# Kernel tuning notes

Hardware: AMD Instinct MI355X
Metric: run time of the kernel (lower is better)

Reference implementation:

```python
import jax, jax.numpy as jnp
import numpy as np

B, C, H, W = 4, 128, 64, 64
THITA = 1e-4


def conv1x1(x, w, b):
    # 1x1 conv + bias + ReLU; x:[B,Cin,H,W], w:[Cout,Cin], b:[Cout]
    return jax.nn.relu(jnp.einsum('bihw,oi->bohw', x, w) + b[None, :, None, None])


_CONV_SPECS = [
    ('neighbor', 2 * C, 4),
    ('pro_key', C, C), ('pro_val', C, C),
    ('lat_key', C, C), ('lat_val', C, C),
    ('tmp1', C, 2 * C),
    ('now1', C, 2),
    ('now_key', C, C), ('now_val', C, C),
    ('q', C, C), ('k', C, C), ('v', C, C),
]


def setup_inputs() -> dict:
    key = jax.random.key(0)
    ks = jax.random.split(key, 1 + 2 * len(_CONV_SPECS))
    inp = {'event': jax.random.normal(ks[0], (B, 6, H, W), dtype=jnp.float32)}
    i = 1
    for name, o, c in _CONV_SPECS:
        s = 1.0 / np.sqrt(c)
        inp['w_' + name] = jax.random.uniform(ks[i], (o, c), minval=-s, maxval=s, dtype=jnp.float32)
        inp['b_' + name] = jax.random.uniform(ks[i + 1], (o,), minval=-s, maxval=s, dtype=jnp.float32)
        i += 2
    return inp


def reference(event, w_neighbor, b_neighbor, w_pro_key, b_pro_key, w_pro_val, b_pro_val,
              w_lat_key, b_lat_key, w_lat_val, b_lat_val, w_tmp1, b_tmp1,
              w_now1, b_now1, w_now_key, b_now_key, w_now_val, b_now_val,
              w_q, b_q, w_k, b_k, w_v, b_v):
    pro, now, lat = event[:, 0:2], event[:, 2:4], event[:, 4:6]
    neigh = conv1x1(jnp.concatenate([pro, lat], axis=1), w_neighbor, b_neighbor)  # [B,2C,H,W]
    pro_key = conv1x1(neigh[:, :C], w_pro_key, b_pro_key)
    pro_val = conv1x1(neigh[:, C:], w_pro_val, b_pro_val)
    lat_key = conv1x1(neigh[:, :C], w_lat_key, b_lat_key)
    lat_val = conv1x1(neigh[:, C:], w_lat_val, b_lat_val)
    # NOTE: source applies conv_tmp1 (shared weights) to both key and val paths
    key_n = conv1x1(jnp.concatenate([pro_key, lat_key], axis=1), w_tmp1, b_tmp1)
    val_n = conv1x1(jnp.concatenate([pro_val, lat_val], axis=1), w_tmp1, b_tmp1)
    now_f = conv1x1(now, w_now1, b_now1)
    now_key = conv1x1(now_f, w_now_key, b_now_key)
    now_val = conv1x1(now_f, w_now_val, b_now_val)
    N = H * W
    q = conv1x1(key_n, w_q, b_q).reshape(B, C, N)          # proj_query pre-permute
    k = conv1x1(now_key, w_k, b_k).reshape(B, C, N)        # [B,C,N]
    attn = jax.nn.softmax(jnp.einsum('bcn,bcm->bnm', q, k), axis=-1)  # [B,N,N]
    v = conv1x1(val_n, w_v, b_v).reshape(B, C, N)
    out = jnp.einsum('bcm,bnm->bcn', v, attn).reshape(B, C, H, W)
    return THITA * out + now_val
```

## Files before the change

### kernel.cpp

```cpp
#include <hip/hip_runtime.h>

#define B_ 4
#define C_ 128
#define N_ 4096
#define LOG2E 1.44269504088896340736f

typedef __attribute__((ext_vector_type(8))) __bf16 bf16x8;
typedef __attribute__((ext_vector_type(16))) float f32x16;

#define SWZ(n) (((n) & 15) << 4)

__device__ __forceinline__ unsigned short cvb(float x) {
    return __builtin_bit_cast(unsigned short, (__bf16)x);
}
__device__ __forceinline__ unsigned pk2(float lo, float hi) {
    return (unsigned)cvb(lo) | ((unsigned)cvb(hi) << 16);
}
__device__ __forceinline__ float bfu(unsigned short u) {
    return __builtin_bit_cast(float, (unsigned)u << 16);
}
__device__ __forceinline__ float fexp2(float x) {
#if __has_builtin(__builtin_amdgcn_exp2f)
    return __builtin_amdgcn_exp2f(x);
#else
    float r;
    asm("v_exp_f32 %0, %1" : "=v"(r) : "v"(x));
    return r;
#endif
}
__device__ inline void gload_lds16(const void* g, void* l) {
    __builtin_amdgcn_global_load_lds(
        (const __attribute__((address_space(1))) unsigned int*)g,
        (__attribute__((address_space(3))) unsigned int*)l, 16, 0, 0);
}
__device__ __forceinline__ void plswapf(float& a, float& b) {
    asm volatile("v_permlane32_swap_b32 %0, %1" : "+v"(a), "+v"(b));
}
__device__ __forceinline__ void plswapu(unsigned& a, unsigned& b) {
    asm volatile("v_permlane32_swap_b32 %0, %1" : "+v"(a), "+v"(b));
}

__global__ __launch_bounds__(256) void k_wcvt(
        const float* pk, const float* lk, const float* pv, const float* lv,
        const float* t1, const float* nk, const float* nv,
        const float* q, const float* k, const float* v,
        const float* bpk, const float* blk, const float* bpv, const float* blv,
        const float* bnk, const float* bnv,
        unsigned short* Wk, unsigned short* Wv, unsigned short* Wt1,
        unsigned short* Wnow, unsigned short* Wq, unsigned short* Wkk,
        unsigned short* Wvv, float* bck, float* bcv, float* bcn) {
    int i = blockIdx.x * 256 + threadIdx.x;
    if      (i < 16384)  Wk[i] = cvb(pk[i]);
    else if (i < 32768)  Wk[i] = cvb(lk[i - 16384]);
    else if (i < 49152)  Wv[i - 32768] = cvb(pv[i - 32768]);
    else if (i < 65536)  Wv[i - 32768] = cvb(lv[i - 49152]);
    else if (i < 98304)  Wt1[i - 65536] = cvb(t1[i - 65536]);
    else if (i < 114688) Wnow[i - 98304] = cvb(nk[i - 98304]);
    else if (i < 131072) Wnow[i - 98304] = cvb(nv[i - 114688]);
    else if (i < 147456) Wq[i - 131072] = cvb(q[i - 131072]);
    else if (i < 163840) Wkk[i - 147456] = cvb(k[i - 147456]);
    else if (i < 180224) Wvv[i - 163840] = cvb(v[i - 163840]);
    else if (i < 180480) { int j = i - 180224; bck[j] = j < 128 ? bpk[j] : blk[j - 128]; }
    else if (i < 180736) { int j = i - 180480; bcv[j] = j < 128 ? bpv[j] : blv[j - 128]; }
    else if (i < 180992) { int j = i - 180736; bcn[j] = j < 128 ? bnk[j] : bnv[j - 128]; }
}

template<int KSTEPS, int ROWB>
__device__ __forceinline__ f32x16 gtile(const char* Ab, int aChBase,
        const unsigned short* W, int Wld, int wrow0, int nsub, int nl, int h) {
    f32x16 acc;
    #pragma unroll
    for (int r = 0; r < 16; ++r) acc[r] = 0.f;
    int n = nsub * 32 + nl;
    const char* arow = Ab + n * ROWB;
    const unsigned short* wrow = W + (size_t)(wrow0 + nl) * Wld + h * 8;
    #pragma unroll
    for (int kk = 0; kk < KSTEPS; ++kk) {
        bf16x8 a = *(const bf16x8*)(arow + ((aChBase + kk * 32 + h * 16) ^ SWZ(n)));
        bf16x8 wf = *(const bf16x8*)(wrow + kk * 16);
        acc = __builtin_amdgcn_mfma_f32_32x32x16_bf16(a, wf, acc, 0, 0, 0);
    }
    return acc;
}

__device__ __forceinline__ void epi_lds(char* dst, int rowB, f32x16 acc,
        const float* bias, int m0, int nsub, int nl, int h) {
    int m = m0 + nl;
    float bs = bias[m];
    #pragma unroll
    for (int r = 0; r < 16; ++r) {
        int n = nsub * 32 + (r & 3) + 8 * (r >> 2) + 4 * h;
        *(unsigned short*)(dst + n * rowB + ((m * 2) ^ SWZ(n))) =
            cvb(fmaxf(acc[r] + bs, 0.f));
    }
}

__device__ __forceinline__ void epi_nc(unsigned short* Y, f32x16 acc,
        const float* bias, float scale, int m0, int nsub, int n0g, int b, int nl, int h) {
    int m = m0 + nl;
    float bs = bias[m];
    #pragma unroll
    for (int r = 0; r < 16; ++r) {
        int n = nsub * 32 + (r & 3) + 8 * (r >> 2) + 4 * h;
        Y[((size_t)b * N_ + n0g + n) * C_ + m] = cvb(fmaxf(acc[r] + bs, 0.f) * scale);
    }
}

__device__ __forceinline__ void epi_cn_b16(unsigned short* Y, f32x16 acc,
        const float* bias, int m0, int nsub, int n0g, int b, int nl, int h) {
    int m = m0 + nl;
    float bs = bias[m];
    #pragma unroll
    for (int r2 = 0; r2 < 4; ++r2) {
        int nn = nsub * 32 + 8 * r2 + 4 * h;
        uint2 o;
        o.x = pk2(fmaxf(acc[4*r2+0] + bs, 0.f), fmaxf(acc[4*r2+1] + bs, 0.f));
        o.y = pk2(fmaxf(acc[4*r2+2] + bs, 0.f), fmaxf(acc[4*r2+3] + bs, 0.f));
        *(uint2*)(Y + ((size_t)b * C_ + m) * N_ + n0g + nn) = o;
    }
}

__device__ __forceinline__ void epi_cn_f32(float* Y, f32x16 acc,
        const float* bias, int m0, int nsub, int n0g, int b, int nl, int h) {
    int m = m0 + nl;
    float bs = bias[m];
    #pragma unroll
    for (int r2 = 0; r2 < 4; ++r2) {
        int nn = nsub * 32 + 8 * r2 + 4 * h;
        float4 o;
        o.x = fmaxf(acc[4*r2+0] + bs, 0.f);
        o.y = fmaxf(acc[4*r2+1] + bs, 0.f);
        o.z = fmaxf(acc[4*r2+2] + bs, 0.f);
        o.w = fmaxf(acc[4*r2+3] + bs, 0.f);
        *(float4*)(Y + ((size_t)b * C_ + m) * N_ + n0g + nn) = o;
    }
}

__global__ __launch_bounds__(512) void k_chain(
        const float* __restrict__ ev, const float* __restrict__ w_nb,
        const float* __restrict__ b_nb, const float* __restrict__ w_n1,
        const float* __restrict__ b_n1,
        const unsigned short* __restrict__ Wk, const unsigned short* __restrict__ Wv,
        const unsigned short* __restrict__ Wt1, const unsigned short* __restrict__ Wnow,
        const unsigned short* __restrict__ Wq, const unsigned short* __restrict__ Wkk,
        const unsigned short* __restrict__ Wvv,
        const float* __restrict__ bck, const float* __restrict__ bcv,
        const float* __restrict__ bt1, const float* __restrict__ bcn,
        const float* __restrict__ bq, const float* __restrict__ bk,
        const float* __restrict__ bv,
        unsigned short* __restrict__ Qt, unsigned short* __restrict__ Kb,
        unsigned short* __restrict__ Vb, float* __restrict__ NowV) {
    __shared__ char lds[114688];
    char* NEIGH = lds;
    char* KCAT  = lds + 32768;
    char* VCAT  = lds + 65536;
    char* NOWF  = lds + 98304;
    char* KEYN  = lds;
    char* VALN  = lds + 16384;
    char* NOWK  = lds + 32768;

    const int t = threadIdx.x, lane = t & 63, w = t >> 6;
    const int nl = lane & 31, h = lane >> 5;
    const int b = blockIdx.y;
    const int n0g = blockIdx.x * 64;

    {
        int n = t & 63, grp = t >> 6;
        const float* evb = ev + (size_t)b * 6 * N_ + n0g + n;
        float e0 = evb[0], e1 = evb[N_], e4 = evb[4*N_], e5 = evb[5*N_];
        float e2 = evb[2*N_], e3 = evb[3*N_];
        int och0 = grp * 32;
        #pragma unroll
        for (int i = 0; i < 32; i += 4) {
            float r_[4];
            #pragma unroll
            for (int j = 0; j < 4; ++j) {
                int o = och0 + i + j;
                float4 w4 = *(const float4*)(w_nb + o * 4);
                r_[j] = fmaxf(b_nb[o] + w4.x*e0 + w4.y*e1 + w4.z*e4 + w4.w*e5, 0.f);
            }
            uint2 val; val.x = pk2(r_[0], r_[1]); val.y = pk2(r_[2], r_[3]);
            *(uint2*)(NEIGH + n * 512 + (((och0 + i) * 2) ^ SWZ(n))) = val;
        }
        int o0 = grp * 16;
        #pragma unroll
        for (int i = 0; i < 16; i += 4) {
            float r_[4];
            #pragma unroll
            for (int j = 0; j < 4; ++j) {
                int o = o0 + i + j;
                float2 w2 = *(const float2*)(w_n1 + o * 2);
                r_[j] = fmaxf(b_n1[o] + w2.x*e2 + w2.y*e3, 0.f);
            }
            uint2 val; val.x = pk2(r_[0], r_[1]); val.y = pk2(r_[2], r_[3]);
            *(uint2*)(NOWF + n * 256 + (((o0 + i) * 2) ^ SWZ(n))) = val;
        }
    }
    __syncthreads();

    {
        int nsub = w & 1, m0 = (w >> 1) * 32;
        f32x16 a0 = gtile<8, 512>(NEIGH, 0,   Wk, 128, m0,       nsub, nl, h);
        f32x16 a1 = gtile<8, 512>(NEIGH, 0,   Wk, 128, m0 + 128, nsub, nl, h);
        f32x16 a2 = gtile<8, 512>(NEIGH, 256, Wv, 128, m0,       nsub, nl, h);
        f32x16 a3 = gtile<8, 512>(NEIGH, 256, Wv, 128, m0 + 128, nsub, nl, h);
        epi_lds(KCAT, 512, a0, bck, m0,       nsub, nl, h);
        epi_lds(KCAT, 512, a1, bck, m0 + 128, nsub, nl, h);
        epi_lds(VCAT, 512, a2, bcv, m0,       nsub, nl, h);
        epi_lds(VCAT, 512, a3, bcv, m0 + 128, nsub, nl, h);
    }
    __syncthreads();

    {
        int nsub = w & 1, m0 = (w >> 1) * 32;
        f32x16 a0 = gtile<16, 512>(KCAT, 0, Wt1, 256, m0, nsub, nl, h);
        f32x16 a1 = gtile<16, 512>(VCAT, 0, Wt1, 256, m0, nsub, nl, h);
        epi_lds(KEYN, 256, a0, bt1, m0, nsub, nl, h);
        epi_lds(VALN, 256, a1, bt1, m0, nsub, nl, h);
    }
    __syncthreads();

    {
        int nsub = w & 1, m0 = (w >> 1) * 32;
        f32x16 a0 = gtile<8, 256>(NOWF, 0, Wnow, 128, m0,       nsub, nl, h);
        f32x16 a1 = gtile<8, 256>(NOWF, 0, Wnow, 128, m0 + 128, nsub, nl, h);
        epi_lds(NOWK, 256, a0, bcn, m0, nsub, nl, h);
        epi_cn_f32(NowV, a1, bcn + 128, m0, nsub, n0g, b, nl, h);
    }
    __syncthreads();

    {
        int nsub = w & 1, m0 = (w >> 1) * 32;
        f32x16 aq = gtile<8, 256>(KEYN, 0, Wq,  128, m0, nsub, nl, h);
        f32x16 ak = gtile<8, 256>(NOWK, 0, Wkk, 128, m0, nsub, nl, h);
        f32x16 av = gtile<8, 256>(VALN, 0, Wvv, 128, m0, nsub, nl, h);
        epi_nc(Qt, aq, bq, LOG2E, m0, nsub, n0g, b, nl, h);
        epi_nc(Kb, ak, bk, 1.0f,  m0, nsub, n0g, b, nl, h);
        epi_cn_b16(Vb, av, bv, m0, nsub, n0g, b, nl, h);
    }
}

#define SPLIT 4
#define CHUNK 32

__global__ __launch_bounds__(128) void k_flashp(
        const unsigned short* __restrict__ Qt, const unsigned short* __restrict__ Kt,
        const unsigned short* __restrict__ Vb,
        unsigned short* __restrict__ Opb, float* __restrict__ ML) {
    __shared__ char stg[2][16384];
    const int t = threadIdx.x;
    const int lane = t & 63;
    const int nh = t >> 6;
    const int h = lane >> 5, nl = lane & 31;
    const int i_ = blockIdx.x;
    const int mpb = (i_ & 7) + 8 * ((i_ >> 3) & 1);
    const int ntile = i_ >> 4;
    const int mp = mpb >> 2, b = mpb & 3;
    const int n0 = ntile * 64 + nh * 32;
    const size_t bo = (size_t)b * N_ * C_;

    bf16x8 qf[8];
    {
        const char* qb = (const char*)(Qt + bo);
        #pragma unroll
        for (int kk = 0; kk < 8; ++kk)
            qf[kk] = *(const bf16x8*)(qb + (size_t)(n0 + nl) * 256 + kk*32 + h*16);
    }

    const char* ktb = (const char*)(Kt + bo);
    const char* vbb = (const char*)(Vb + bo);

    f32x16 oa[4];
    #pragma unroll
    for (int ss = 0; ss < 4; ++ss)
        #pragma unroll
        for (int r = 0; r < 16; ++r) oa[ss][r] = 0.f;
    float m_run = -1e30f, l_run = 0.f;

    const int swzK = (nl & 15) << 4;
    const int swzV = ((nl >> 1) & 7) << 4;

    auto stage = [&](int tile, int ph) {
        char* base = stg[ph];
        if (nh == 0) {
            const char* src = ktb + (size_t)tile * 8192;
            #pragma unroll
            for (int ii = 0; ii < 8; ++ii) {
                int L = ii*1024 + lane*16;
                int T = L ^ (((L >> 8) & 15) << 4);
                gload_lds16(src + T, base + ii*1024);
            }
        } else {
            const char* src = vbb + (size_t)tile * 64;
            #pragma unroll
            for (int ii = 0; ii < 8; ++ii) {
                int L = ii*1024 + lane*16;
                int T = L ^ (((L >> 7) & 7) << 4);
                int c = T >> 6, inner = T & 63;
                gload_lds16(src + (size_t)c * (N_*2) + inner, base + 8192 + ii*1024);
            }
        }
    };

    const int tb = mp * CHUNK;
    stage(tb, 0);
    stage(tb + 1, 1);

    for (int it = 0; it < CHUNK; ++it) {
        int ph = it & 1;
        if (it < CHUNK - 1) asm volatile("s_waitcnt vmcnt(8)" ::: "memory");
        else                asm volatile("s_waitcnt vmcnt(0)" ::: "memory");
        __builtin_amdgcn_s_barrier();
        __builtin_amdgcn_sched_barrier(0);
        const char* kb = stg[ph];
        const char* vb = kb + 8192;

        f32x16 s;
        #pragma unroll
        for (int r = 0; r < 16; ++r) s[r] = 0.f;
        __builtin_amdgcn_s_setprio(1);
        #pragma unroll
        for (int kk = 0; kk < 8; ++kk) {
            int y = nl*256 + kk*32 + h*16;
            bf16x8 a = *(const bf16x8*)(kb + (y ^ swzK));
            s = __builtin_amdgcn_mfma_f32_32x32x16_bf16(a, qf[kk], s, 0, 0, 0);
        }
        __builtin_amdgcn_s_setprio(0);

        float tm = fmaxf(fmaxf(fmaxf(s[0], s[1]), fmaxf(s[2], s[3])),
                         fmaxf(fmaxf(s[4], s[5]), fmaxf(s[6], s[7])));
        float tm2 = fmaxf(fmaxf(fmaxf(s[8], s[9]), fmaxf(s[10], s[11])),
                          fmaxf(fmaxf(s[12], s[13]), fmaxf(s[14], s[15])));
        tm = fmaxf(tm, tm2);
        { float x = tm, y = tm; plswapf(x, y); tm = fmaxf(x, y); }
        if (!__all(tm <= m_run + 8.f)) {
            float mn = fmaxf(m_run, tm);
            float sc = fexp2(m_run - mn);
            m_run = mn;
            l_run *= sc;
            #pragma unroll
            for (int ss = 0; ss < 4; ++ss)
                #pragma unroll
                for (int r = 0; r < 16; ++r) oa[ss][r] *= sc;
        }
        float p[16];
        float ls = 0.f;
        #pragma unroll
        for (int r = 0; r < 16; ++r) { p[r] = fexp2(s[r] - m_run); ls += p[r]; }
        { float x = ls, y = ls; plswapf(x, y); ls = x + y; }
        l_run += ls;

        unsigned pk_[8];
        #pragma unroll
        for (int q = 0; q < 8; ++q) pk_[q] = pk2(p[2*q], p[2*q+1]);
        unsigned a0 = pk_[0], a1 = pk_[1], b0 = pk_[2], b1 = pk_[3];
        plswapu(a0, b0); plswapu(a1, b1);
        unsigned c0 = pk_[4], c1 = pk_[5], d0 = pk_[6], d1 = pk_[7];
        plswapu(c0, d0); plswapu(c1, d1);
        typedef __attribute__((ext_vector_type(4))) unsigned u32x4;
        u32x4 uw0 = {a0, a1, b0, b1};
        u32x4 uw1 = {c0, c1, d0, d1};
        bf16x8 pf0 = __builtin_bit_cast(bf16x8, uw0);
        bf16x8 pf1 = __builtin_bit_cast(bf16x8, uw1);

        __builtin_amdgcn_s_setprio(1);
        #pragma unroll
        for (int ss = 0; ss < 4; ++ss) {
            int y0 = (32*ss + nl)*64 + h*16;
            bf16x8 va0 = *(const bf16x8*)(vb + (y0 ^ swzV));
            oa[ss] = __builtin_amdgcn_mfma_f32_32x32x16_bf16(va0, pf0, oa[ss], 0, 0, 0);
            bf16x8 va1 = *(const bf16x8*)(vb + ((y0 + 32) ^ swzV));
            oa[ss] = __builtin_amdgcn_mfma_f32_32x32x16_bf16(va1, pf1, oa[ss], 0, 0, 0);
        }
        __builtin_amdgcn_s_setprio(0);

        __builtin_amdgcn_sched_barrier(0);
        __builtin_amdgcn_s_barrier();
        if (it + 2 < CHUNK) stage(tb + it + 2, ph);
    }

    const size_t pb = (size_t)(mp * B_ + b) * 64 + ntile;
    if (h == 0) {
        ML[pb*128 +      nh*32 + nl] = m_run;
        ML[pb*128 + 64 + nh*32 + nl] = l_run;
    }
    unsigned short* dst = Opb + pb * 8192;
    #pragma unroll
    for (int ss = 0; ss < 4; ++ss)
        #pragma unroll
        for (int r = 0; r < 16; ++r) {
            int c = 32*ss + (r&3) + 8*(r>>2) + 4*h;
            dst[c*64 + nh*32 + nl] = cvb(oa[ss][r]);
        }
}

__global__ __launch_bounds__(256) void k_comb(const unsigned short* __restrict__ Opb,
        const float* __restrict__ ML, const float* __restrict__ NV,
        float* __restrict__ out) {
    const int t = threadIdx.x;
    const int ntile = blockIdx.x, b = blockIdx.y;
    const int n = t & 63, tq = t >> 6;
    float mj[SPLIT], lj[SPLIT], wj[SPLIT];
    #pragma unroll
    for (int j = 0; j < SPLIT; ++j) {
        size_t pb = (size_t)(j * B_ + b) * 64 + ntile;
        mj[j] = ML[pb*128 + n];
        lj[j] = ML[pb*128 + 64 + n];
    }
    float M = fmaxf(fmaxf(mj[0], mj[1]), fmaxf(mj[2], mj[3]));
    float den = 0.f;
    #pragma unroll
    for (int j = 0; j < SPLIT; ++j) { wj[j] = fexp2(mj[j] - M); den += lj[j] * wj[j]; }
    float sc = 1e-4f / den;
    #pragma unroll 4
    for (int c = tq; c < C_; c += 4) {
        float v = 0.f;
        #pragma unroll
        for (int j = 0; j < SPLIT; ++j)
            v += bfu(Opb[((size_t)(j * B_ + b) * 64 + ntile) * 8192 + c*64 + n]) * wj[j];
        size_t gi = ((size_t)b * C_ + c) * N_ + ntile*64 + n;
        out[gi] = sc * v + NV[gi];
    }
}

extern "C" void kernel_launch(void* const* d_in, const int* in_sizes, int n_in,
                              void* d_out, int out_size, void* d_ws, size_t ws_size,
                              hipStream_t stream) {
    const float* ev   = (const float*)d_in[0];
    const float* w_nb = (const float*)d_in[1];  const float* b_nb = (const float*)d_in[2];
    const float* w_pk = (const float*)d_in[3];  const float* b_pk = (const float*)d_in[4];
    const float* w_pv = (const float*)d_in[5];  const float* b_pv = (const float*)d_in[6];
    const float* w_lk = (const float*)d_in[7];  const float* b_lk = (const float*)d_in[8];
    const float* w_lv = (const float*)d_in[9];  const float* b_lv = (const float*)d_in[10];
    const float* w_t1 = (const float*)d_in[11]; const float* b_t1 = (const float*)d_in[12];
    const float* w_n1 = (const float*)d_in[13]; const float* b_n1 = (const float*)d_in[14];
    const float* w_nk = (const float*)d_in[15]; const float* b_nk = (const float*)d_in[16];
    const float* w_nv = (const float*)d_in[17]; const float* b_nv = (const float*)d_in[18];
    const float* w_q  = (const float*)d_in[19]; const float* b_q  = (const float*)d_in[20];
    const float* w_k  = (const float*)d_in[21]; const float* b_k  = (const float*)d_in[22];
    const float* w_v  = (const float*)d_in[23]; const float* b_v  = (const float*)d_in[24];

    char* p = (char*)d_ws;
    unsigned short* Qt = (unsigned short*)p; p += (size_t)B_*N_*C_*2;
    unsigned short* Kb = (unsigned short*)p; p += (size_t)B_*N_*C_*2;
    unsigned short* Vb = (unsigned short*)p; p += (size_t)B_*C_*N_*2;
    float*          NowV = (float*)p;        p += (size_t)B_*C_*N_*4;
    unsigned short* Wk   = (unsigned short*)p; p += 32768*2;
    unsigned short* Wv   = (unsigned short*)p; p += 32768*2;
    unsigned short* Wt1  = (unsigned short*)p; p += 32768*2;
    unsigned short* Wnow = (unsigned short*)p; p += 32768*2;
    unsigned short* Wq   = (unsigned short*)p; p += 16384*2;
    unsigned short* Wkk  = (unsigned short*)p; p += 16384*2;
    unsigned short* Wvv  = (unsigned short*)p; p += 16384*2;
    float* bck = (float*)p; p += 256*4;
    float* bcv = (float*)p; p += 256*4;
    float* bcn = (float*)p; p += 256*4;
    p = (char*)(((size_t)p + 255) & ~(size_t)255);
    unsigned short* Opb = (unsigned short*)p; p += (size_t)SPLIT*B_*64*8192*2;
    float* ML = (float*)p; p += (size_t)SPLIT*B_*64*128*4;

    k_wcvt<<<dim3(707), dim3(256), 0, stream>>>(
        w_pk, w_lk, w_pv, w_lv, w_t1, w_nk, w_nv, w_q, w_k, w_v,
        b_pk, b_lk, b_pv, b_lv, b_nk, b_nv,
        Wk, Wv, Wt1, Wnow, Wq, Wkk, Wvv, bck, bcv, bcn);

    k_chain<<<dim3(N_/64, B_), dim3(512), 0, stream>>>(
        ev, w_nb, b_nb, w_n1, b_n1,
        Wk, Wv, Wt1, Wnow, Wq, Wkk, Wvv,
        bck, bcv, b_t1, bcn, b_q, b_k, b_v,
        Qt, Kb, Vb, NowV);

    k_flashp<<<dim3(N_/64 * SPLIT * B_), dim3(128), 0, stream>>>(Qt, Kb, Vb, Opb, ML);

    k_comb<<<dim3(N_/64, B_), dim3(256), 0, stream>>>(Opb, ML, NowV, (float*)d_out);
}
```

Baseline: 94.58 us.

## Halve k_chain tile to 32 pixels and double flash split-K to 8

k_chain now handles 32 pixels per block with 256 threads and half the LDS, so it launches twice as many blocks and more of them can be resident at once. The flash attention partial kernel's key/value split rises from 4 to 8 chunks, with a new block-index mapping, to give more blocks and better occupancy. The combine kernel now reduces over SPLIT generically. This adds more partial output traffic and combine work, and each block processes a smaller GEMM tile.

Measured after the change: 114.7 us. +21.2%, slower.

```diff
diff --git a/kernel.cpp b/kernel.cpp
--- a/kernel.cpp
+++ b/kernel.cpp
@@ -67,11 +67,11 @@
 
 template<int KSTEPS, int ROWB>
 __device__ __forceinline__ f32x16 gtile(const char* Ab, int aChBase,
-        const unsigned short* W, int Wld, int wrow0, int nsub, int nl, int h) {
+        const unsigned short* W, int Wld, int wrow0, int nl, int h) {
     f32x16 acc;
     #pragma unroll
     for (int r = 0; r < 16; ++r) acc[r] = 0.f;
-    int n = nsub * 32 + nl;
+    int n = nl;
     const char* arow = Ab + n * ROWB;
     const unsigned short* wrow = W + (size_t)(wrow0 + nl) * Wld + h * 8;
     #pragma unroll
@@ -84,35 +84,35 @@
 }
 
 __device__ __forceinline__ void epi_lds(char* dst, int rowB, f32x16 acc,
-        const float* bias, int m0, int nsub, int nl, int h) {
+        const float* bias, int m0, int nl, int h) {
     int m = m0 + nl;
     float bs = bias[m];
     #pragma unroll
     for (int r = 0; r < 16; ++r) {
-        int n = nsub * 32 + (r & 3) + 8 * (r >> 2) + 4 * h;
+        int n = (r & 3) + 8 * (r >> 2) + 4 * h;
         *(unsigned short*)(dst + n * rowB + ((m * 2) ^ SWZ(n))) =
             cvb(fmaxf(acc[r] + bs, 0.f));
     }
 }
 
 __device__ __forceinline__ void epi_nc(unsigned short* Y, f32x16 acc,
-        const float* bias, float scale, int m0, int nsub, int n0g, int b, int nl, int h) {
+        const float* bias, float scale, int m0, int n0g, int b, int nl, int h) {
     int m = m0 + nl;
     float bs = bias[m];
     #pragma unroll
     for (int r = 0; r < 16; ++r) {
-        int n = nsub * 32 + (r & 3) + 8 * (r >> 2) + 4 * h;
+        int n = (r & 3) + 8 * (r >> 2) + 4 * h;
         Y[((size_t)b * N_ + n0g + n) * C_ + m] = cvb(fmaxf(acc[r] + bs, 0.f) * scale);
     }
 }
 
 __device__ __forceinline__ void epi_cn_b16(unsigned short* Y, f32x16 acc,
-        const float* bias, int m0, int nsub, int n0g, int b, int nl, int h) {
+        const float* bias, int m0, int n0g, int b, int nl, int h) {
     int m = m0 + nl;
     float bs = bias[m];
     #pragma unroll
     for (int r2 = 0; r2 < 4; ++r2) {
-        int nn = nsub * 32 + 8 * r2 + 4 * h;
+        int nn = 8 * r2 + 4 * h;
         uint2 o;
         o.x = pk2(fmaxf(acc[4*r2+0] + bs, 0.f), fmaxf(acc[4*r2+1] + bs, 0.f));
         o.y = pk2(fmaxf(acc[4*r2+2] + bs, 0.f), fmaxf(acc[4*r2+3] + bs, 0.f));
@@ -121,12 +121,12 @@
 }
 
 __device__ __forceinline__ void epi_cn_f32(float* Y, f32x16 acc,
-        const float* bias, int m0, int nsub, int n0g, int b, int nl, int h) {
+        const float* bias, int m0, int n0g, int b, int nl, int h) {
     int m = m0 + nl;
     float bs = bias[m];
     #pragma unroll
     for (int r2 = 0; r2 < 4; ++r2) {
-        int nn = nsub * 32 + 8 * r2 + 4 * h;
+        int nn = 8 * r2 + 4 * h;
         float4 o;
         o.x = fmaxf(acc[4*r2+0] + bs, 0.f);
         o.y = fmaxf(acc[4*r2+1] + bs, 0.f);
@@ -136,7 +136,7 @@
     }
 }
 
-__global__ __launch_bounds__(512) void k_chain(
+__global__ __launch_bounds__(256) void k_chain(
         const float* __restrict__ ev, const float* __restrict__ w_nb,
         const float* __restrict__ b_nb, const float* __restrict__ w_n1,
         const float* __restrict__ b_n1,
@@ -150,22 +150,23 @@
         const float* __restrict__ bv,
         unsigned short* __restrict__ Qt, unsigned short* __restrict__ Kb,
         unsigned short* __restrict__ Vb, float* __restrict__ NowV) {
-    __shared__ char lds[114688];
+    __shared__ char lds[57344];
     char* NEIGH = lds;
-    char* KCAT  = lds + 32768;
-    char* VCAT  = lds + 65536;
-    char* NOWF  = lds + 98304;
+    char* KCAT  = lds + 16384;
+    char* VCAT  = lds + 32768;
+    char* NOWF  = lds + 49152;
     char* KEYN  = lds;
-    char* VALN  = lds + 16384;
-    char* NOWK  = lds + 32768;
+    char* VALN  = lds + 8192;
+    char* NOWK  = lds + 16384;
 
     const int t = threadIdx.x, lane = t & 63, w = t >> 6;
     const int nl = lane & 31, h = lane >> 5;
     const int b = blockIdx.y;
-    const int n0g = blockIdx.x * 64;
-
-    {
-        int n = t & 63, grp = t >> 6;
+    const int n0g = blockIdx.x * 32;
+    const int m0 = w * 32;
+
+    {
+        int n = t & 31, grp = t >> 5;
         const float* evb = ev + (size_t)b * 6 * N_ + n0g + n;
         float e0 = evb[0], e1 = evb[N_], e4 = evb[4*N_], e5 = evb[5*N_];
         float e2 = evb[2*N_], e3 = evb[3*N_];
@@ -199,49 +200,45 @@
     __syncthreads();
 
     {
-        int nsub = w & 1, m0 = (w >> 1) * 32;
-        f32x16 a0 = gtile<8, 512>(NEIGH, 0,   Wk, 128, m0,       nsub, nl, h);
-        f32x16 a1 = gtile<8, 512>(NEIGH, 0,   Wk, 128, m0 + 128, nsub, nl, h);
-        f32x16 a2 = gtile<8, 512>(NEIGH, 256, Wv, 128, m0,       nsub, nl, h);
-        f32x16 a3 = gtile<8, 512>(NEIGH, 256, Wv, 128, m0 + 128, nsub, nl, h);
-        epi_lds(KCAT, 512, a0, bck, m0,       nsub, nl, h);
-        epi_lds(KCAT, 512, a1, bck, m0 + 128, nsub, nl, h);
-        epi_lds(VCAT, 512, a2, bcv, m0,       nsub, nl, h);
-        epi_lds(VCAT, 512, a3, bcv, m0 + 128, nsub, nl, h);
+        f32x16 a0 = gtile<8, 512>(NEIGH, 0,   Wk, 128, m0,       nl, h);
+        f32x16 a1 = gtile<8, 512>(NEIGH, 0,   Wk, 128, m0 + 128, nl, h);
+        f32x16 a2 = gtile<8, 512>(NEIGH, 256, Wv, 128, m0,       nl, h);
+        f32x16 a3 = gtile<8, 512>(NEIGH, 256, Wv, 128, m0 + 128, nl, h);
+        epi_lds(KCAT, 512, a0, bck, m0,       nl, h);
+        epi_lds(KCAT, 512, a1, bck, m0 + 128, nl, h);
+        epi_lds(VCAT, 512, a2, bcv, m0,       nl, h);
+        epi_lds(VCAT, 512, a3, bcv, m0 + 128, nl, h);
     }
     __syncthreads();
 
     {
-        int nsub = w & 1, m0 = (w >> 1) * 32;
-        f32x16 a0 = gtile<16, 512>(KCAT, 0, Wt1, 256, m0, nsub, nl, h);
-        f32x16 a1 = gtile<16, 512>(VCAT, 0, Wt1, 256, m0, nsub, nl, h);
-        epi_lds(KEYN, 256, a0, bt1, m0, nsub, nl, h);
-        epi_lds(VALN, 256, a1, bt1, m0, nsub, nl, h);
+        f32x16 a0 = gtile<16, 512>(KCAT, 0, Wt1, 256, m0, nl, h);
+        f32x16 a1 = gtile<16, 512>(VCAT, 0, Wt1, 256, m0, nl, h);
+        epi_lds(KEYN, 256, a0, bt1, m0, nl, h);
+        epi_lds(VALN, 256, a1, bt1, m0, nl, h);
     }
     __syncthreads();
 
     {
-        int nsub = w & 1, m0 = (w >> 1) * 32;
-        f32x16 a0 = gtile<8, 256>(NOWF, 0, Wnow, 128, m0,       nsub, nl, h);
-        f32x16 a1 = gtile<8, 256>(NOWF, 0, Wnow, 128, m0 + 128, nsub, nl, h);
-        epi_lds(NOWK, 256, a0, bcn, m0, nsub, nl, h);
-        epi_cn_f32(NowV, a1, bcn + 128, m0, nsub, n0g, b, nl, h);
+        f32x16 a0 = gtile<8, 256>(NOWF, 0, Wnow, 128, m0,       nl, h);
+        f32x16 a1 = gtile<8, 256>(NOWF, 0, Wnow, 128, m0 + 128, nl, h);
+        epi_lds(NOWK, 256, a0, bcn, m0, nl, h);
+        epi_cn_f32(NowV, a1, bcn + 128, m0, n0g, b, nl, h);
     }
     __syncthreads();
 
     {
-        int nsub = w & 1, m0 = (w >> 1) * 32;
-        f32x16 aq = gtile<8, 256>(KEYN, 0, Wq,  128, m0, nsub, nl, h);
-        f32x16 ak = gtile<8, 256>(NOWK, 0, Wkk, 128, m0, nsub, nl, h);
-        f32x16 av = gtile<8, 256>(VALN, 0, Wvv, 128, m0, nsub, nl, h);
-        epi_nc(Qt, aq, bq, LOG2E, m0, nsub, n0g, b, nl, h);
-        epi_nc(Kb, ak, bk, 1.0f,  m0, nsub, n0g, b, nl, h);
-        epi_cn_b16(Vb, av, bv, m0, nsub, n0g, b, nl, h);
-    }
-}
-
-#define SPLIT 4
-#define CHUNK 32
+        f32x16 aq = gtile<8, 256>(KEYN, 0, Wq,  128, m0, nl, h);
+        f32x16 ak = gtile<8, 256>(NOWK, 0, Wkk, 128, m0, nl, h);
+        f32x16 av = gtile<8, 256>(VALN, 0, Wvv, 128, m0, nl, h);
+        epi_nc(Qt, aq, bq, LOG2E, m0, n0g, b, nl, h);
+        epi_nc(Kb, ak, bk, 1.0f,  m0, n0g, b, nl, h);
+        epi_cn_b16(Vb, av, bv, m0, n0g, b, nl, h);
+    }
+}
+
+#define SPLIT 8
+#define CHUNK 16
 
 __global__ __launch_bounds__(128) void k_flashp(
         const unsigned short* __restrict__ Qt, const unsigned short* __restrict__ Kt,
@@ -253,9 +250,9 @@
     const int nh = t >> 6;
     const int h = lane >> 5, nl = lane & 31;
     const int i_ = blockIdx.x;
-    const int mpb = (i_ & 7) + 8 * ((i_ >> 3) & 1);
-    const int ntile = i_ >> 4;
-    const int mp = mpb >> 2, b = mpb & 3;
+    const int combo = i_ & 31;
+    const int ntile = i_ >> 5;
+    const int mp = combo >> 2, b = combo & 3;
     const int n0 = ntile * 64 + nh * 32;
     const size_t bo = (size_t)b * N_ * C_;
 
@@ -407,7 +404,9 @@
         mj[j] = ML[pb*128 + n];
         lj[j] = ML[pb*128 + 64 + n];
     }
-    float M = fmaxf(fmaxf(mj[0], mj[1]), fmaxf(mj[2], mj[3]));
+    float M = -1e30f;
+    #pragma unroll
+    for (int j = 0; j < SPLIT; ++j) M = fmaxf(M, mj[j]);
     float den = 0.f;
     #pragma unroll
     for (int j = 0; j < SPLIT; ++j) { wj[j] = fexp2(mj[j] - M); den += lj[j] * wj[j]; }
@@ -464,7 +463,7 @@
         b_pk, b_lk, b_pv, b_lv, b_nk, b_nv,
         Wk, Wv, Wt1, Wnow, Wq, Wkk, Wvv, bck, bcv, bcn);
 
-    k_chain<<<dim3(N_/64, B_), dim3(512), 0, stream>>>(
+    k_chain<<<dim3(N_/32, B_), dim3(256), 0, stream>>>(
         ev, w_nb, b_nb, w_n1, b_n1,
         Wk, Wv, Wt1, Wnow, Wq, Wkk, Wvv,
         bck, bcv, b_t1, bcn, b_q, b_k, b_v,
```
